# Kernel tuning notes

Hardware: AMD Instinct MI355X
Metric: run time of the kernel (lower is better)

## Reference

```python
import jax, jax.numpy as jnp
import numpy as np

TEMP = 0.05
EPS_SOFTMAX = 1e-6
EPS_LOG = 1e-6


def setup_inputs() -> dict:
    key = jax.random.key(0)
    k1, k2, k3, k4, k5 = jax.random.split(key, 5)
    B, F, N, C = 256, 128, 200000, 1000
    inputs = jax.random.normal(k1, (B, F), dtype=jnp.float32)
    inputs_s = jax.random.normal(k2, (B, F), dtype=jnp.float32)
    features = jax.random.normal(k3, (N, F), dtype=jnp.float32)
    # memory banks are kept L2-normalized (see MB.backward renorm)
    features = features / jnp.linalg.norm(features, axis=1, keepdims=True)
    labels = jax.random.randint(k4, (N,), 0, C, dtype=jnp.int64)
    indexes = jax.random.randint(k5, (B,), 0, N, dtype=jnp.int64)
    return {"inputs": inputs, "inputs_s": inputs_s, "features": features,
            "labels": labels, "indexes": indexes, "k": 10, "num_classes": C}


def reference(inputs, inputs_s, features, labels, indexes, k, num_classes):
    B = inputs.shape[0]
    N = features.shape[0]
    # features is a buffer (no grad in torch); MB backward also treats it as constant
    feats = jax.lax.stop_gradient(features)

    # MB.forward: inputs @ features.T, then /temp  -> [B, N]
    inputs_out = (inputs @ feats.T) / TEMP

    # local similarity [B, B]
    local = inputs @ inputs_s.T
    # topk neighbors in the bank, gather + per-sample bmm, sum over k -> [B, 1]
    _, nb_idx = jax.lax.top_k(inputs_out, k)          # [B, k]
    nb_ftr = feats[nb_idx]                             # [B, k, F]
    _local = jnp.einsum('bf,bkf->b', inputs, nb_ftr)[:, None]  # [B, 1]
    # (local + _local) masked to diagonal, then /temp
    local = (local + _local) * jnp.eye(B, dtype=local.dtype)
    local = local / TEMP

    targets = labels[indexes]                          # [B]

    # label-bucketed segment reductions -> sim [C, B]
    sim = jax.ops.segment_sum(inputs_out.T, labels, num_segments=num_classes)
    sim = sim + jax.ops.segment_sum(local, targets, num_segments=num_classes)

    nums = jax.ops.segment_sum(jnp.ones((N, 1), jnp.float32), labels,
                               num_segments=num_classes)        # [C, 1]
    nums_help = jax.ops.segment_sum(jnp.ones((B, 1), jnp.float32), targets,
                                    num_segments=num_classes)   # [C, 1]
    nums = nums + (nums_help > 0).astype(jnp.float32) * (k + 1)

    mask = (nums > 0).astype(jnp.float32)              # [C, 1]
    sim = sim / (mask * nums + (1.0 - mask))           # broadcast over B

    # masked softmax over classes, per sample: vec [B, C], mask [1, C]
    vec = sim.T
    m = mask.T                                          # [1, C]
    exps = jnp.exp(vec) * m
    masked_sim = exps / (jnp.sum(exps, axis=1, keepdims=True) + EPS_SOFTMAX)

    logp = jnp.log(masked_sim + EPS_LOG)
    loss = -jnp.mean(logp[jnp.arange(B), targets])
    return loss
```

## Files before the change

kernel.cpp:

```cpp
#include <hip/hip_runtime.h>

#define CMAX 1024
#define BQ 256
#define FQ 128
#define TN 64
#define QCAP 128

typedef __attribute__((ext_vector_type(8))) short bf16x8;
typedef __attribute__((ext_vector_type(4))) float f32x4;

__device__ __forceinline__ unsigned short f2bf(float f){
  unsigned u = __float_as_uint(f);
  unsigned r = (u + 0x7FFFu + ((u >> 16) & 1u)) >> 16;
  return (unsigned short)r;
}
__device__ __forceinline__ unsigned encf(float f){
  unsigned u = __float_as_uint(f);
  return (u & 0x80000000u) ? ~u : (u | 0x80000000u);
}
__device__ __forceinline__ void ins16(float (&d)[16], float v){
  #pragma unroll
  for (int j = 15; j > 0; --j) d[j] = fminf(d[j-1], fmaxf(v, d[j]));
  d[0] = fmaxf(v, d[0]);
}

__global__ void k_prep(const float* __restrict__ inputs, const float* __restrict__ inputs_s,
                       const int* __restrict__ labels, const int* __restrict__ indexes,
                       unsigned short* __restrict__ inputs_bf,
                       int* __restrict__ cnt, int* __restrict__ numsh,
                       int* __restrict__ targets, float* __restrict__ diag,
                       float* __restrict__ thr, int N)
{
  int idx = blockIdx.x*blockDim.x + threadIdx.x;
  int stride = gridDim.x*blockDim.x;
  for (int n = idx; n < N; n += stride) atomicAdd(&cnt[labels[n]], 1);
  for (int i = idx; i < BQ*FQ; i += stride) inputs_bf[i] = f2bf(inputs[i]);
  if (blockIdx.x == 0){
    int t = threadIdx.x;
    int tg = labels[indexes[t]];
    targets[t] = tg;
    atomicAdd(&numsh[tg], 1);
    float s = 0.f, s2 = 0.f;
    const float4* a = (const float4*)(inputs + t*FQ);
    const float4* b = (const float4*)(inputs_s + t*FQ);
    #pragma unroll
    for (int f = 0; f < FQ/4; ++f){
      float4 x = a[f], y = b[f];
      s  += x.x*y.x + x.y*y.y + x.z*y.z + x.w*y.w;
      s2 += x.x*x.x + x.y*x.y + x.z*x.z + x.w*x.w;
    }
    diag[t] = s;
    thr[t] = 3.05f * sqrtf(s2 * (1.0f/128.0f));
  }
}

__global__ void k_scan(const int* __restrict__ cnt, int* __restrict__ cur,
                       const int* __restrict__ cptr)
{
  __shared__ int s[CMAX];
  int C = cptr[0]; if (C > CMAX) C = CMAX;
  int t = threadIdx.x;
  s[t] = (t < C) ? cnt[t] : 0;
  __syncthreads();
  for (int off = 1; off < CMAX; off <<= 1){
    int v = s[t] + ((t >= off) ? s[t - off] : 0);
    __syncthreads();
    s[t] = v;
    __syncthreads();
  }
  if (t < C) cur[t] = s[t] - cnt[t];
}

__global__ void k_scatter(const int* __restrict__ labels, int* __restrict__ cur,
                          int* __restrict__ sorted_idx, int* __restrict__ sorted_cls, int N)
{
  int idx = blockIdx.x*blockDim.x + threadIdx.x;
  int stride = gridDim.x*blockDim.x;
  for (int n = idx; n < N; n += stride){
    int c = labels[n];
    int pos = atomicAdd(&cur[c], 1);
    sorted_idx[pos] = n;
    sorted_cls[pos] = c;
  }
}

__global__ __launch_bounds__(256, 3) void k_main(
    const float* __restrict__ feats,
    const int* __restrict__ sorted_idx,
    const int* __restrict__ sorted_cls,
    const unsigned short* __restrict__ inputs_bf,
    const float* __restrict__ thr,
    float* __restrict__ sim,
    float* __restrict__ topk_ws,
    int N, int NCHUNK)
{
  __shared__ unsigned short fl[TN*FQ];
  __shared__ int idx_s[TN];
  __shared__ int cls_s[TN];
  __shared__ unsigned q_lds[4][QCAP];
  __shared__ int qn_lds[4];

  const int t = threadIdx.x;
  const int lane = t & 63;
  const int w = t >> 6;
  const int c16 = lane & 15;
  const int g = lane >> 4;
  const int g4 = g * 4;
  const int b0 = w * 64;

  float thrs[4];
  #pragma unroll
  for (int bt = 0; bt < 4; ++bt) thrs[bt] = thr[b0 + bt*16 + c16];

  float d[16];
  #pragma unroll
  for (int j = 0; j < 16; ++j) d[j] = -INFINITY;

  for (int chunk = blockIdx.x; chunk < NCHUNK; chunk += gridDim.x){
    const int base = chunk * TN;
    const int valid = min(TN, N - base);

    if (t < TN){
      idx_s[t] = (t < valid) ? sorted_idx[base + t] : 0;
      cls_s[t] = (t < valid) ? sorted_cls[base + t] : -1;
    }
    __syncthreads();

    {
      const int i = t >> 2, q = t & 3;
      const float4* src = (const float4*)(feats + (size_t)idx_s[i] * FQ);
      #pragma unroll
      for (int j = 0; j < 8; ++j){
        float4 v;
        if (i < valid) v = src[j*4 + q];
        else { v.x = v.y = v.z = v.w = 0.f; }
        int h0 = (j*16 + q*4) ^ ((i & 7) << 3);
        ushort4 u;
        u.x = f2bf(v.x); u.y = f2bf(v.y); u.z = f2bf(v.z); u.w = f2bf(v.w);
        *(ushort4*)&fl[i*FQ + h0] = u;
      }
      if (lane == 0) qn_lds[w] = 0;
    }
    __syncthreads();

    f32x4 acc[4][4];
    #pragma unroll
    for (int nt = 0; nt < 4; ++nt)
      #pragma unroll
      for (int bt = 0; bt < 4; ++bt)
        acc[nt][bt] = (f32x4){0.f, 0.f, 0.f, 0.f};
    #pragma unroll
    for (int ks = 0; ks < 4; ++ks){
      bf16x8 af[4], bfr[4];
      #pragma unroll
      for (int nt = 0; nt < 4; ++nt){
        int r = nt*16 + c16;
        int h = r*FQ + ((ks*32 + g*8) ^ ((r & 7) << 3));
        af[nt] = *(const bf16x8*)&fl[h];
      }
      #pragma unroll
      for (int bt = 0; bt < 4; ++bt){
        int b = b0 + bt*16 + c16;
        bfr[bt] = *(const bf16x8*)&inputs_bf[b*FQ + ks*32 + g*8];
      }
      #pragma unroll
      for (int nt = 0; nt < 4; ++nt)
        #pragma unroll
        for (int bt = 0; bt < 4; ++bt)
          acc[nt][bt] = __builtin_amdgcn_mfma_f32_16x16x32_bf16(af[nt], bfr[bt], acc[nt][bt], 0, 0, 0);
    }

    unsigned long long bmask = __ballot((lane < TN-1) && (cls_s[lane] != cls_s[lane+1]));

    #pragma unroll
    for (int bt = 0; bt < 4; ++bt){
      float smax = -INFINITY;
      #pragma unroll
      for (int nt = 0; nt < 4; ++nt)
        #pragma unroll
        for (int r = 0; r < 4; ++r)
          smax = fmaxf(smax, acc[nt][bt][r]);
      if (__any(smax > thrs[bt])){
        if (smax > thrs[bt]){
          #pragma unroll
          for (int nt = 0; nt < 4; ++nt)
            #pragma unroll
            for (int r = 0; r < 4; ++r){
              float v = acc[nt][bt][r];
              if (v > thrs[bt]){
                int pos = atomicAdd(&qn_lds[w], 1);
                if (pos < QCAP)
                  q_lds[w][pos] = (__float_as_uint(v) & 0xFFFFFF00u) | (unsigned)(bt*16 + c16);
              }
            }
        }
      }
    }

    float red[4];
    if (bmask == 0ull){
      #pragma unroll
      for (int bt = 0; bt < 4; ++bt){
        float ssum = 0.f;
        #pragma unroll
        for (int nt = 0; nt < 4; ++nt)
          #pragma unroll
          for (int r = 0; r < 4; ++r)
            ssum += acc[nt][bt][r];
        ssum += __shfl_xor(ssum, 16, 64);
        ssum += __shfl_xor(ssum, 32, 64);
        red[bt] = ssum;
      }
      float mysum = red[0];
      if (g == 1) mysum = red[1];
      if (g == 2) mysum = red[2];
      if (g == 3) mysum = red[3];
      int c = cls_s[0];
      if (c >= 0) atomicAdd(&sim[c*BQ + b0 + lane], mysum);
    } else {
      unsigned long long m = bmask;
      int lo = 0;
      while (lo < TN){
        int hi = m ? (int)__builtin_ffsll((long long)m) : TN;
        #pragma unroll
        for (int bt = 0; bt < 4; ++bt){
          float ssum = 0.f;
          #pragma unroll
          for (int nt = 0; nt < 4; ++nt)
            #pragma unroll
            for (int r = 0; r < 4; ++r){
              int n = nt*16 + g4 + r;
              ssum += ((n >= lo) && (n < hi)) ? acc[nt][bt][r] : 0.f;
            }
          ssum += __shfl_xor(ssum, 16, 64);
          ssum += __shfl_xor(ssum, 32, 64);
          red[bt] = ssum;
        }
        float mysum = red[0];
        if (g == 1) mysum = red[1];
        if (g == 2) mysum = red[2];
        if (g == 3) mysum = red[3];
        int c = cls_s[lo];
        if (c >= 0) atomicAdd(&sim[c*BQ + b0 + lane], mysum);
        lo = hi; m &= (m - 1);
      }
    }

    __builtin_amdgcn_wave_barrier();
    asm volatile("s_waitcnt lgkmcnt(0)" ::: "memory");
    int qn = qn_lds[w];
    if (qn > QCAP) qn = QCAP;
    for (int qi = 0; qi < qn; ++qi){
      unsigned pk = q_lds[w][qi];
      if ((int)(pk & 0xFFu) == lane){
        float v = __uint_as_float(pk & 0xFFFFFF00u);
        if (v > d[15]) ins16(d, v);
      }
    }
    __syncthreads();
  }

  #pragma unroll
  for (int j = 0; j < 16; ++j)
    topk_ws[((size_t)blockIdx.x*BQ + t)*16 + j] = d[j];
}

__global__ void k_merge(const float* __restrict__ topk_ws, int NB,
                        const float* __restrict__ diag, const int* __restrict__ targets,
                        float* __restrict__ sim, const int* __restrict__ kptr)
{
  __shared__ float Ld[4][64][16];
  const int t = threadIdx.x;
  const int lane = t & 63;
  const int w = t >> 6;
  const int b = blockIdx.x*4 + w;

  float d[16];
  #pragma unroll
  for (int j = 0; j < 16; ++j) d[j] = -INFINITY;
  for (int bk = lane; bk < NB; bk += 64){
    const float* src = topk_ws + ((size_t)bk*BQ + b)*16;
    for (int j = 0; j < 16; ++j){
      float v = src[j];
      if (!(v > d[15])) break;
      ins16(d, v);
    }
  }
  #pragma unroll
  for (int j = 0; j < 16; ++j) Ld[w][lane][j] = d[j];
  __syncthreads();
  int kk = kptr[0]; if (kk > 16) kk = 16;
  int h = 0;
  float myhead = Ld[w][lane][0];
  float tops = 0.f;
  for (int p = 0; p < 16; ++p){
    unsigned pk = (encf(myhead) & 0xFFFFFFC0u) | (unsigned)lane;
    #pragma unroll
    for (int s = 32; s > 0; s >>= 1){
      unsigned o = (unsigned)__shfl_xor((int)pk, s, 64);
      pk = (o > pk) ? o : pk;
    }
    int wl = (int)(pk & 63u);
    float val = __shfl(myhead, wl, 64);
    if (p < kk) tops += val;
    if (lane == wl){
      ++h;
      myhead = (h < 16) ? Ld[w][lane][h] : -INFINITY;
    }
  }
  if (lane == 0){
    atomicAdd(&sim[targets[b]*BQ + b], diag[b] + tops);
  }
}

__global__ void k_expsum(const float* __restrict__ sim, const int* __restrict__ cnt,
                         const int* __restrict__ numsh, const int* __restrict__ targets,
                         const int* __restrict__ kptr, const int* __restrict__ cptr,
                         float* __restrict__ esum, float* __restrict__ etgt)
{
  int t = threadIdx.x;
  int C = cptr[0]; if (C > CMAX) C = CMAX;
  int kk = kptr[0];
  int tgt = targets[t];
  float local = 0.f;
  const float invT = 20.0f;
  for (int c = blockIdx.x; c < C; c += gridDim.x){
    float nums = (float)cnt[c] + ((numsh[c] > 0) ? (float)(kk + 1) : 0.f);
    float denom = (nums > 0.f) ? nums : 1.f;
    float val = sim[c*BQ + t] * invT / denom;
    float e = (nums > 0.f) ? expf(val) : 0.f;
    local += e;
    if (c == tgt) etgt[t] = e;
  }
  atomicAdd(&esum[t], local);
}

__global__ void k_loss(const float* __restrict__ esum, const float* __restrict__ etgt,
                       float* __restrict__ out)
{
  __shared__ float red[BQ];
  int t = threadIdx.x;
  float p = etgt[t] / (esum[t] + 1e-6f);
  float l = -logf(p + 1e-6f);
  red[t] = l;
  __syncthreads();
  for (int off = 128; off > 0; off >>= 1){
    if (t < off) red[t] += red[t + off];
    __syncthreads();
  }
  if (t == 0) out[0] = red[0] / 256.0f;
}

extern "C" void kernel_launch(void* const* d_in, const int* in_sizes, int n_in,
                              void* d_out, int out_size, void* d_ws, size_t ws_size,
                              hipStream_t stream) {
  const float* inputs   = (const float*)d_in[0];
  const float* inputs_s = (const float*)d_in[1];
  const float* feats    = (const float*)d_in[2];
  const int*   labels   = (const int*)d_in[3];
  const int*   indexes  = (const int*)d_in[4];
  const int*   kptr     = (const int*)d_in[5];
  const int*   cptr     = (const int*)d_in[6];
  const int N = in_sizes[3];

  char* ws = (char*)d_ws;
  int*      cnt       = (int*)(ws + 0);
  int*      numsh     = (int*)(ws + 4096);
  float*    esum      = (float*)(ws + 8192);
  float*    etgt      = (float*)(ws + 9216);
  float*    sim       = (float*)(ws + 16384);
  int*      targets   = (int*)(ws + 1064960);
  float*    diag      = (float*)(ws + 1065984);
  float*    thr       = (float*)(ws + 1067008);
  int*      cur       = (int*)(ws + 1068032);
  unsigned short* inputs_bf = (unsigned short*)(ws + 1072128);
  int*      sorted_idx = (int*)(ws + 1137664);
  int*      sorted_cls = sorted_idx + N;
  size_t off_topk = (1137664 + 8*(size_t)N + 255) & ~(size_t)255;
  float*    topk      = (float*)(ws + off_topk);

  const int NCHUNK = (N + TN - 1) / TN;
  int NB = 768;
  if (NB > NCHUNK) NB = NCHUNK;
  long long topk_cap = ((long long)ws_size - (long long)off_topk) / (BQ*16*4);
  if (topk_cap < NB) NB = (int)topk_cap;
  if (NB < 1) NB = 1;
  int gN = (N + 255) / 256; if (gN > 512) gN = 512; if (gN < 1) gN = 1;

  hipMemsetAsync(ws, 0, 1064960, stream);
  k_prep<<<gN, 256, 0, stream>>>(inputs, inputs_s, labels, indexes, inputs_bf,
                                 cnt, numsh, targets, diag, thr, N);
  k_scan<<<1, 1024, 0, stream>>>(cnt, cur, cptr);
  k_scatter<<<gN, 256, 0, stream>>>(labels, cur, sorted_idx, sorted_cls, N);
  k_main<<<NB, 256, 0, stream>>>(feats, sorted_idx, sorted_cls, inputs_bf, thr,
                                 sim, topk, N, NCHUNK);
  k_merge<<<BQ/4, 256, 0, stream>>>(topk, NB, diag, targets, sim, kptr);
  k_expsum<<<64, 256, 0, stream>>>(sim, cnt, numsh, targets, kptr, cptr, esum, etgt);
  k_loss<<<1, 256, 0, stream>>>(esum, etgt, (float*)d_out);
}
```

Measured before the change: 219.1 us.

## Partition main kernel by class boundaries with prefetched double-buffered feature tiles

Each block of the main kernel now takes a contiguous range of whole classes in sorted order, found by binary search over class start offsets. Per-class sums are carried across tiles in registers and written to sim with plain stores, which removes the global atomics and the large sim memset. The next tile's feature rows are loaded into registers while the current tile is converted and processed, using two LDS buffers. The label histogram in the prep kernel moves to shared memory. The risks are load imbalance from uneven class-aligned ranges, and uninitialised sim entries for classes that no block writes.

```diff
diff --git a/kernel.cpp b/kernel.cpp
--- a/kernel.cpp
+++ b/kernel.cpp
@@ -5,6 +5,7 @@
 #define FQ 128
 #define TN 64
 #define QCAP 128
+#define NBLK_DEF 768
 
 typedef __attribute__((ext_vector_type(8))) short bf16x8;
 typedef __attribute__((ext_vector_type(4))) float f32x4;
@@ -31,12 +32,20 @@
                        int* __restrict__ targets, float* __restrict__ diag,
                        float* __restrict__ thr, int N)
 {
-  int idx = blockIdx.x*blockDim.x + threadIdx.x;
-  int stride = gridDim.x*blockDim.x;
-  for (int n = idx; n < N; n += stride) atomicAdd(&cnt[labels[n]], 1);
+  __shared__ int h[CMAX];
+  int t = threadIdx.x;
+  for (int c = t; c < CMAX; c += 256) h[c] = 0;
+  __syncthreads();
+  int idx = blockIdx.x*256 + t;
+  int stride = gridDim.x*256;
+  for (int n = idx; n < N; n += stride) atomicAdd(&h[labels[n]], 1);
   for (int i = idx; i < BQ*FQ; i += stride) inputs_bf[i] = f2bf(inputs[i]);
-  if (blockIdx.x == 0){
-    int t = threadIdx.x;
+  __syncthreads();
+  for (int c = t; c < CMAX; c += 256){
+    int v = h[c];
+    if (v) atomicAdd(&cnt[c], v);
+  }
+  if (blockIdx.x == 0 && t < BQ){
     int tg = labels[indexes[t]];
     targets[t] = tg;
     atomicAdd(&numsh[tg], 1);
@@ -55,7 +64,7 @@
 }
 
 __global__ void k_scan(const int* __restrict__ cnt, int* __restrict__ cur,
-                       const int* __restrict__ cptr)
+                       int* __restrict__ pstart, const int* __restrict__ cptr)
 {
   __shared__ int s[CMAX];
   int C = cptr[0]; if (C > CMAX) C = CMAX;
@@ -68,7 +77,12 @@
     s[t] = v;
     __syncthreads();
   }
-  if (t < C) cur[t] = s[t] - cnt[t];
+  if (t < C){
+    int e = s[t] - cnt[t];
+    cur[t] = e;
+    pstart[t] = e;
+  }
+  if (t == C-1) pstart[C] = s[t];
 }
 
 __global__ void k_scatter(const int* __restrict__ labels, int* __restrict__ cur,
@@ -90,13 +104,13 @@
     const int* __restrict__ sorted_cls,
     const unsigned short* __restrict__ inputs_bf,
     const float* __restrict__ thr,
+    const int* __restrict__ pstart,
     float* __restrict__ sim,
     float* __restrict__ topk_ws,
-    int N, int NCHUNK)
-{
-  __shared__ unsigned short fl[TN*FQ];
-  __shared__ int idx_s[TN];
-  __shared__ int cls_s[TN];
+    const int* __restrict__ cptr,
+    int N, int nblk)
+{
+  __shared__ unsigned short fl[2][TN*FQ];
   __shared__ unsigned q_lds[4][QCAP];
   __shared__ int qn_lds[4];
 
@@ -107,162 +121,206 @@
   const int g = lane >> 4;
   const int g4 = g * 4;
   const int b0 = w * 64;
-
-  float thrs[4];
-  #pragma unroll
-  for (int bt = 0; bt < 4; ++bt) thrs[bt] = thr[b0 + bt*16 + c16];
+  const int rowoff = t >> 2;
+  const int q = t & 3;
 
   float d[16];
   #pragma unroll
-  for (int j = 0; j < 16; ++j) d[j] = -INFINITY;
-
-  for (int chunk = blockIdx.x; chunk < NCHUNK; chunk += gridDim.x){
-    const int base = chunk * TN;
-    const int valid = min(TN, N - base);
-
-    if (t < TN){
-      idx_s[t] = (t < valid) ? sorted_idx[base + t] : 0;
-      cls_s[t] = (t < valid) ? sorted_cls[base + t] : -1;
-    }
-    __syncthreads();
-
+  for (int i2 = 0; i2 < 16; ++i2) d[i2] = -INFINITY;
+
+  int C = cptr[0]; if (C > CMAX) C = CMAX;
+  const int j = blockIdx.x;
+  const int Tj  = (int)(((long long)j * N) / nblk);
+  const int Tj1 = (int)(((long long)(j+1) * N) / nblk);
+  int lo = 0, hi = C;
+  while (lo < hi){ int mid = (lo+hi)>>1; if (pstart[mid] < Tj) lo = mid+1; else hi = mid; }
+  const int c_lo = lo;
+  hi = C;
+  while (lo < hi){ int mid = (lo+hi)>>1; if (pstart[mid] < Tj1) lo = mid+1; else hi = mid; }
+  const int c_hi = lo;
+  const int e_lo = pstart[c_lo];
+  const int e_hi = pstart[c_hi];
+
+  if (e_lo < e_hi){
+    float thrs[4];
+    #pragma unroll
+    for (int bt = 0; bt < 4; ++bt) thrs[bt] = thr[b0 + bt*16 + c16];
+    float racc[4] = {0.f, 0.f, 0.f, 0.f};
+    if (lane == 0) qn_lds[w] = 0;
+
+    const int nch = (e_hi - e_lo + TN - 1) / TN;
+
+    int myrow = e_lo + rowoff;
+    int idx_cur = (myrow < e_hi) ? sorted_idx[myrow] : 0;
+    float4 f[8];
     {
-      const int i = t >> 2, q = t & 3;
-      const float4* src = (const float4*)(feats + (size_t)idx_s[i] * FQ);
+      const float4* src = (const float4*)(feats + (size_t)idx_cur * FQ);
       #pragma unroll
-      for (int j = 0; j < 8; ++j){
-        float4 v;
-        if (i < valid) v = src[j*4 + q];
-        else { v.x = v.y = v.z = v.w = 0.f; }
-        int h0 = (j*16 + q*4) ^ ((i & 7) << 3);
-        ushort4 u;
-        u.x = f2bf(v.x); u.y = f2bf(v.y); u.z = f2bf(v.z); u.w = f2bf(v.w);
-        *(ushort4*)&fl[i*FQ + h0] = u;
-      }
-      if (lane == 0) qn_lds[w] = 0;
-    }
-    __syncthreads();
-
-    f32x4 acc[4][4];
-    #pragma unroll
-    for (int nt = 0; nt < 4; ++nt)
+      for (int jj = 0; jj < 8; ++jj) f[jj] = src[jj*4 + q];
+    }
+    int idx_nxt = (myrow + TN < e_hi) ? sorted_idx[myrow + TN] : 0;
+
+    for (int m = 0; m < nch; ++m){
+      const int base = e_lo + m*TN;
+      const int valid = min(TN, e_hi - base);
+      unsigned short* flb = fl[m & 1];
+
+      {
+        const bool live = (rowoff < valid);
+        #pragma unroll
+        for (int jj = 0; jj < 8; ++jj){
+          float4 v = f[jj];
+          if (!live){ v.x = 0.f; v.y = 0.f; v.z = 0.f; v.w = 0.f; }
+          int h0 = (jj*16 + q*4) ^ ((rowoff & 7) << 3);
+          ushort4 u;
+          u.x = f2bf(v.x); u.y = f2bf(v.y); u.z = f2bf(v.z); u.w = f2bf(v.w);
+          *(ushort4*)&flb[rowoff*FQ + h0] = u;
+        }
+      }
+      if (m + 1 < nch){
+        const float4* src = (const float4*)(feats + (size_t)idx_nxt * FQ);
+        #pragma unroll
+        for (int jj = 0; jj < 8; ++jj) f[jj] = src[jj*4 + q];
+        int r2 = base + 2*TN + rowoff;
+        idx_nxt = (r2 < e_hi) ? sorted_idx[r2] : 0;
+      }
+      const int mypos = base + lane;
+      const int myc  = (mypos < e_hi)     ? sorted_cls[mypos]     : -1;
+      const int mync = (mypos + 1 < e_hi) ? sorted_cls[mypos + 1] : -2;
+      const unsigned long long bmask = __ballot((lane < valid) && (myc != mync));
+
+      __syncthreads();
+
+      f32x4 acc[4][4];
       #pragma unroll
-      for (int bt = 0; bt < 4; ++bt)
-        acc[nt][bt] = (f32x4){0.f, 0.f, 0.f, 0.f};
-    #pragma unroll
-    for (int ks = 0; ks < 4; ++ks){
-      bf16x8 af[4], bfr[4];
+      for (int nt = 0; nt < 4; ++nt)
+        #pragma unroll
+        for (int bt = 0; bt < 4; ++bt)
+          acc[nt][bt] = (f32x4){0.f, 0.f, 0.f, 0.f};
       #pragma unroll
-      for (int nt = 0; nt < 4; ++nt){
-        int r = nt*16 + c16;
-        int h = r*FQ + ((ks*32 + g*8) ^ ((r & 7) << 3));
-        af[nt] = *(const bf16x8*)&fl[h];
-      }
+      for (int ks = 0; ks < 4; ++ks){
+        bf16x8 af[4], bfr[4];
+        #pragma unroll
+        for (int nt = 0; nt < 4; ++nt){
+          int r = nt*16 + c16;
+          int h = r*FQ + ((ks*32 + g*8) ^ ((r & 7) << 3));
+          af[nt] = *(const bf16x8*)&flb[h];
+        }
+        #pragma unroll
+        for (int bt = 0; bt < 4; ++bt){
+          int b = b0 + bt*16 + c16;
+          bfr[bt] = *(const bf16x8*)&inputs_bf[b*FQ + ks*32 + g*8];
+        }
+        #pragma unroll
+        for (int nt = 0; nt < 4; ++nt)
+          #pragma unroll
+          for (int bt = 0; bt < 4; ++bt)
+            acc[nt][bt] = __builtin_amdgcn_mfma_f32_16x16x32_bf16(af[nt], bfr[bt], acc[nt][bt], 0, 0, 0);
+      }
+
       #pragma unroll
       for (int bt = 0; bt < 4; ++bt){
-        int b = b0 + bt*16 + c16;
-        bfr[bt] = *(const bf16x8*)&inputs_bf[b*FQ + ks*32 + g*8];
-      }
-      #pragma unroll
-      for (int nt = 0; nt < 4; ++nt)
-        #pragma unroll
-        for (int bt = 0; bt < 4; ++bt)
-          acc[nt][bt] = __builtin_amdgcn_mfma_f32_16x16x32_bf16(af[nt], bfr[bt], acc[nt][bt], 0, 0, 0);
-    }
-
-    unsigned long long bmask = __ballot((lane < TN-1) && (cls_s[lane] != cls_s[lane+1]));
-
-    #pragma unroll
-    for (int bt = 0; bt < 4; ++bt){
-      float smax = -INFINITY;
-      #pragma unroll
-      for (int nt = 0; nt < 4; ++nt)
-        #pragma unroll
-        for (int r = 0; r < 4; ++r)
-          smax = fmaxf(smax, acc[nt][bt][r]);
-      if (__any(smax > thrs[bt])){
-        if (smax > thrs[bt]){
+        float smax = -INFINITY;
+        #pragma unroll
+        for (int nt = 0; nt < 4; ++nt)
+          #pragma unroll
+          for (int r = 0; r < 4; ++r)
+            smax = fmaxf(smax, acc[nt][bt][r]);
+        if (__any(smax > thrs[bt])){
+          if (smax > thrs[bt]){
+            #pragma unroll
+            for (int nt = 0; nt < 4; ++nt)
+              #pragma unroll
+              for (int r = 0; r < 4; ++r){
+                float v = acc[nt][bt][r];
+                if (v > thrs[bt]){
+                  int pos = atomicAdd(&qn_lds[w], 1);
+                  if (pos < QCAP)
+                    q_lds[w][pos] = (__float_as_uint(v) & 0xFFFFFF00u) | (unsigned)(bt*16 + c16);
+                }
+              }
+          }
+        }
+      }
+
+      if (bmask == 0ull){
+        #pragma unroll
+        for (int bt = 0; bt < 4; ++bt){
+          float ss = 0.f;
           #pragma unroll
           for (int nt = 0; nt < 4; ++nt)
             #pragma unroll
-            for (int r = 0; r < 4; ++r){
-              float v = acc[nt][bt][r];
-              if (v > thrs[bt]){
-                int pos = atomicAdd(&qn_lds[w], 1);
-                if (pos < QCAP)
-                  q_lds[w][pos] = (__float_as_uint(v) & 0xFFFFFF00u) | (unsigned)(bt*16 + c16);
+            for (int r = 0; r < 4; ++r)
+              ss += acc[nt][bt][r];
+          ss += __shfl_xor(ss, 16, 64);
+          ss += __shfl_xor(ss, 32, 64);
+          racc[bt] += ss;
+        }
+      } else {
+        int seglo = 0;
+        unsigned long long mm = bmask;
+        while (mm){
+          const int p = (int)__builtin_ctzll(mm);
+          float s4[4];
+          #pragma unroll
+          for (int bt = 0; bt < 4; ++bt){
+            float ss = 0.f;
+            #pragma unroll
+            for (int nt = 0; nt < 4; ++nt)
+              #pragma unroll
+              for (int r = 0; r < 4; ++r){
+                int n = nt*16 + g4 + r;
+                ss += ((n >= seglo) && (n <= p)) ? acc[nt][bt][r] : 0.f;
               }
-            }
-        }
-      }
-    }
-
-    float red[4];
-    if (bmask == 0ull){
-      #pragma unroll
-      for (int bt = 0; bt < 4; ++bt){
-        float ssum = 0.f;
-        #pragma unroll
-        for (int nt = 0; nt < 4; ++nt)
-          #pragma unroll
-          for (int r = 0; r < 4; ++r)
-            ssum += acc[nt][bt][r];
-        ssum += __shfl_xor(ssum, 16, 64);
-        ssum += __shfl_xor(ssum, 32, 64);
-        red[bt] = ssum;
-      }
-      float mysum = red[0];
-      if (g == 1) mysum = red[1];
-      if (g == 2) mysum = red[2];
-      if (g == 3) mysum = red[3];
-      int c = cls_s[0];
-      if (c >= 0) atomicAdd(&sim[c*BQ + b0 + lane], mysum);
-    } else {
-      unsigned long long m = bmask;
-      int lo = 0;
-      while (lo < TN){
-        int hi = m ? (int)__builtin_ffsll((long long)m) : TN;
+            ss += __shfl_xor(ss, 16, 64);
+            ss += __shfl_xor(ss, 32, 64);
+            if (seglo == 0) ss += racc[bt];
+            s4[bt] = ss;
+          }
+          const int c = __shfl(myc, p, 64);
+          if (g == 0){
+            #pragma unroll
+            for (int bt = 0; bt < 4; ++bt)
+              sim[(size_t)c*BQ + b0 + bt*16 + c16] = s4[bt];
+          }
+          seglo = p + 1;
+          mm &= mm - 1;
+        }
         #pragma unroll
         for (int bt = 0; bt < 4; ++bt){
-          float ssum = 0.f;
+          float ss = 0.f;
           #pragma unroll
           for (int nt = 0; nt < 4; ++nt)
             #pragma unroll
             for (int r = 0; r < 4; ++r){
               int n = nt*16 + g4 + r;
-              ssum += ((n >= lo) && (n < hi)) ? acc[nt][bt][r] : 0.f;
+              ss += (n >= seglo) ? acc[nt][bt][r] : 0.f;
             }
-          ssum += __shfl_xor(ssum, 16, 64);
-          ssum += __shfl_xor(ssum, 32, 64);
-          red[bt] = ssum;
-        }
-        float mysum = red[0];
-        if (g == 1) mysum = red[1];
-        if (g == 2) mysum = red[2];
-        if (g == 3) mysum = red[3];
-        int c = cls_s[lo];
-        if (c >= 0) atomicAdd(&sim[c*BQ + b0 + lane], mysum);
-        lo = hi; m &= (m - 1);
-      }
-    }
-
-    __builtin_amdgcn_wave_barrier();
-    asm volatile("s_waitcnt lgkmcnt(0)" ::: "memory");
-    int qn = qn_lds[w];
-    if (qn > QCAP) qn = QCAP;
-    for (int qi = 0; qi < qn; ++qi){
-      unsigned pk = q_lds[w][qi];
-      if ((int)(pk & 0xFFu) == lane){
-        float v = __uint_as_float(pk & 0xFFFFFF00u);
-        if (v > d[15]) ins16(d, v);
-      }
-    }
-    __syncthreads();
+          ss += __shfl_xor(ss, 16, 64);
+          ss += __shfl_xor(ss, 32, 64);
+          racc[bt] = ss;
+        }
+      }
+
+      __builtin_amdgcn_wave_barrier();
+      asm volatile("s_waitcnt lgkmcnt(0)" ::: "memory");
+      int qn = qn_lds[w];
+      if (qn > QCAP) qn = QCAP;
+      for (int qi = 0; qi < qn; ++qi){
+        unsigned pk = q_lds[w][qi];
+        if ((int)(pk & 0xFFu) == lane){
+          float v = __uint_as_float(pk & 0xFFFFFF00u);
+          if (v > d[15]) ins16(d, v);
+        }
+      }
+      __builtin_amdgcn_wave_barrier();
+      if (lane == 0) qn_lds[w] = 0;
+    }
   }
 
   #pragma unroll
-  for (int j = 0; j < 16; ++j)
-    topk_ws[((size_t)blockIdx.x*BQ + t)*16 + j] = d[j];
+  for (int i2 = 0; i2 < 16; ++i2)
+    topk_ws[((size_t)blockIdx.x*BQ + t)*16 + i2] = d[i2];
 }
 
 __global__ void k_merge(const float* __restrict__ topk_ws, int NB,
@@ -309,7 +367,7 @@
     }
   }
   if (lane == 0){
-    atomicAdd(&sim[targets[b]*BQ + b], diag[b] + tops);
+    atomicAdd(&sim[(size_t)targets[b]*BQ + b], diag[b] + tops);
   }
 }
 
@@ -327,7 +385,7 @@
   for (int c = blockIdx.x; c < C; c += gridDim.x){
     float nums = (float)cnt[c] + ((numsh[c] > 0) ? (float)(kk + 1) : 0.f);
     float denom = (nums > 0.f) ? nums : 1.f;
-    float val = sim[c*BQ + t] * invT / denom;
+    float val = sim[(size_t)c*BQ + t] * invT / denom;
     float e = (nums > 0.f) ? expf(val) : 0.f;
     local += e;
     if (c == tgt) etgt[t] = e;
@@ -368,33 +426,32 @@
   int*      numsh     = (int*)(ws + 4096);
   float*    esum      = (float*)(ws + 8192);
   float*    etgt      = (float*)(ws + 9216);
-  float*    sim       = (float*)(ws + 16384);
-  int*      targets   = (int*)(ws + 1064960);
-  float*    diag      = (float*)(ws + 1065984);
-  float*    thr       = (float*)(ws + 1067008);
-  int*      cur       = (int*)(ws + 1068032);
-  unsigned short* inputs_bf = (unsigned short*)(ws + 1072128);
-  int*      sorted_idx = (int*)(ws + 1137664);
+  int*      targets   = (int*)(ws + 10240);
+  float*    diag      = (float*)(ws + 11264);
+  float*    thr       = (float*)(ws + 12288);
+  int*      cur       = (int*)(ws + 13312);
+  int*      pstart    = (int*)(ws + 17408);
+  unsigned short* inputs_bf = (unsigned short*)(ws + 21760);
+  float*    sim       = (float*)(ws + 87296);
+  int*      sorted_idx = (int*)(ws + 1135872);
   int*      sorted_cls = sorted_idx + N;
-  size_t off_topk = (1137664 + 8*(size_t)N + 255) & ~(size_t)255;
+  size_t off_topk = (1135872 + 8*(size_t)N + 255) & ~(size_t)255;
   float*    topk      = (float*)(ws + off_topk);
 
-  const int NCHUNK = (N + TN - 1) / TN;
-  int NB = 768;
-  if (NB > NCHUNK) NB = NCHUNK;
+  int nblk = NBLK_DEF;
   long long topk_cap = ((long long)ws_size - (long long)off_topk) / (BQ*16*4);
-  if (topk_cap < NB) NB = (int)topk_cap;
-  if (NB < 1) NB = 1;
-  int gN = (N + 255) / 256; if (gN > 512) gN = 512; if (gN < 1) gN = 1;
-
-  hipMemsetAsync(ws, 0, 1064960, stream);
-  k_prep<<<gN, 256, 0, stream>>>(inputs, inputs_s, labels, indexes, inputs_bf,
+  if (topk_cap < nblk) nblk = (int)topk_cap;
+  if (nblk < 1) nblk = 1;
+  int gN = (N + 255) / 256; if (gN > 128) gN = 128; if (gN < 1) gN = 1;
+
+  hipMemsetAsync(ws, 0, 10240, stream);
+  k_prep<<<64, 256, 0, stream>>>(inputs, inputs_s, labels, indexes, inputs_bf,
                                  cnt, numsh, targets, diag, thr, N);
-  k_scan<<<1, 1024, 0, stream>>>(cnt, cur, cptr);
+  k_scan<<<1, 1024, 0, stream>>>(cnt, cur, pstart, cptr);
   k_scatter<<<gN, 256, 0, stream>>>(labels, cur, sorted_idx, sorted_cls, N);
-  k_main<<<NB, 256, 0, stream>>>(feats, sorted_idx, sorted_cls, inputs_bf, thr,
-                                 sim, topk, N, NCHUNK);
-  k_merge<<<BQ/4, 256, 0, stream>>>(topk, NB, diag, targets, sim, kptr);
+  k_main<<<nblk, 256, 0, stream>>>(feats, sorted_idx, sorted_cls, inputs_bf, thr,
+                                   pstart, sim, topk, cptr, N, nblk);
+  k_merge<<<BQ/4, 256, 0, stream>>>(topk, nblk, diag, targets, sim, kptr);
   k_expsum<<<64, 256, 0, stream>>>(sim, cnt, numsh, targets, kptr, cptr, esum, etgt);
   k_loss<<<1, 256, 0, stream>>>(esum, etgt, (float*)d_out);
 }
```

Result: slower. 246.5 us (+12.5%).
